# Optimization experiments

Hardware: AMD Instinct MI355X
Metric: run time of the kernel (lower is better)

The kernel has to match this reference:

```python
import jax, jax.numpy as jnp
import numpy as np

UNITS = 65
BATCH = 50
SEQ = 8192


def setup_inputs() -> dict:
    key = jax.random.key(0)
    ks = jax.random.split(key, 6)
    x = jax.random.normal(ks[0], (BATCH, SEQ, UNITS), dtype=jnp.float32)
    # Single shared LSTM cell (same cell object reused for all 3 stacked layers)
    W = jax.random.normal(ks[1], (UNITS, 4 * UNITS), dtype=jnp.float32) * 0.1
    U = jax.random.normal(ks[2], (UNITS, 4 * UNITS), dtype=jnp.float32) * 0.1
    b = jax.random.normal(ks[3], (4 * UNITS,), dtype=jnp.float32) * 0.1
    # Dense output projection 65 -> 65
    Wd = jax.random.normal(ks[4], (UNITS, UNITS), dtype=jnp.float32) * 0.1
    bd = jax.random.normal(ks[5], (UNITS,), dtype=jnp.float32) * 0.1
    return {"x": x, "W": W, "U": U, "b": b, "Wd": Wd, "bd": bd}


def _lstm_cell(x_t, h, c, W, U, b):
    # Keras LSTMCell: gates in order i, f, g(candidate), o
    z = x_t @ W + h @ U + b                      # [B, 4*units]
    i, f, g, o = jnp.split(z, 4, axis=-1)
    i = jax.nn.sigmoid(i)
    f = jax.nn.sigmoid(f)
    g = jnp.tanh(g)
    o = jax.nn.sigmoid(o)
    c_new = f * c + i * g
    h_new = o * jnp.tanh(c_new)
    return h_new, c_new


def reference(x, W, U, b, Wd, bd):
    B = x.shape[0]
    zeros = jnp.zeros((B, UNITS), dtype=x.dtype)
    init = (zeros, zeros, zeros, zeros, zeros, zeros)  # (h1,c1,h2,c2,h3,c3)

    def step(carry, x_t):
        h1, c1, h2, c2, h3, c3 = carry
        h1, c1 = _lstm_cell(x_t, h1, c1, W, U, b)  # layer 1 (shared weights)
        h2, c2 = _lstm_cell(h1, h2, c2, W, U, b)   # layer 2 (shared weights)
        h3, c3 = _lstm_cell(h2, h3, c3, W, U, b)   # layer 3 (shared weights)
        return (h1, c1, h2, c2, h3, c3), h3

    xs = jnp.swapaxes(x, 0, 1)                   # [T, B, 65]
    _, ys = jax.lax.scan(step, init, xs)         # ys: [T, B, 65]
    ys = jnp.swapaxes(ys, 0, 1)                  # [B, T, 65]
    out = ys @ Wd + bd                           # dense projection to vocab 65
    return out
```

## Files before the change

### kernel.cpp

```cpp
#include <hip/hip_runtime.h>

#define UNITS 65
#define SEQ   8192
#define BATCH 50

__device__ __forceinline__ float frcp(float x){ return __builtin_amdgcn_rcpf(x); }
__device__ __forceinline__ float fsigmoid(float x){ return frcp(1.0f + __expf(-x)); }
__device__ __forceinline__ float ftanh(float x){
    float e2 = __expf(2.0f * x);
    return 1.0f - 2.0f * frcp(e2 + 1.0f);
}

template<int CTRL>
__device__ __forceinline__ float dppadd(float x){
    int t = __builtin_amdgcn_update_dpp(0, __float_as_int(x), CTRL, 0xF, 0xF, true);
    return x + __int_as_float(t);
}
template<int CTRL>
__device__ __forceinline__ float dppmov(float x){
    int t = __builtin_amdgcn_update_dpp(0, __float_as_int(x), CTRL, 0xF, 0xF, true);
    return __int_as_float(t);
}
__device__ __forceinline__ float red4_all(float x){
    x = dppadd<0xB1>(x);
    x = dppadd<0x4E>(x);
    return x;
}
__device__ __forceinline__ float swzadd_xor4(float x){
    int t = __builtin_amdgcn_ds_swizzle(__float_as_int(x), 0x101F);
    return x + __int_as_float(t);
}
__device__ __forceinline__ float red8_all(float x){
    return swzadd_xor4(red4_all(x));
}
__device__ __forceinline__ float red16_lane15(float x){
    x = dppadd<0x111>(x);
    x = dppadd<0x112>(x);
    x = dppadd<0x114>(x);
    x = dppadd<0x118>(x);
    return x;
}
__device__ __forceinline__ void bar_lds(){
    asm volatile("s_waitcnt lgkmcnt(0)\n\ts_barrier" ::: "memory");
}
__device__ __forceinline__ float rdlane(float v, int l){
    return __int_as_float(__builtin_amdgcn_readlane(__float_as_int(v), l));
}

__device__ __forceinline__ int inpos8(int k){
    return (k < 112) ? ((k >> 4) * 20 + (k & 15)) : (140 + (k - 112));
}
__device__ __forceinline__ float wrow(const float* W, const float* U, int k, int c){
    return (k < 65) ? W[k * 260 + c] : U[(k - 65) * 260 + c];
}


#define LAYERB(aI, aF, aG, aO, CST, ...) do {                                  \
    float rI_ = red8_all(aI), rF_ = red8_all(aF);                              \
    float rG_ = red8_all(aG), rO_ = red8_all(aO);                              \
    float z_ = ((gate == 0) ? rI_ : (gate == 1) ? rF_ : (gate == 2) ? rG_ : rO_) + breg; \
    float sg_ = frcp(1.0f + __expf(-sk * z_));                                 \
    float g_  = fmaf(sk, sg_, dk);                                             \
    float gi_ = dppmov<0x00>(g_);                                              \
    float gf_ = dppmov<0x55>(g_);                                              \
    float gg_ = dppmov<0xAA>(g_);                                              \
    float cn_ = fmaf(gf_, CST, gi_ * gg_);                                     \
    float hn_ = g_ * ftanh(cn_);                                               \
    if (wr) { CST = cn_; __VA_ARGS__; }                                        \
} while (0)

#define STEP(L0, L1, L2, VB, NB) do {                                          \
    const float* __restrict__ vbase = (VB);                                    \
    float*       __restrict__ nbase = (NB);                                    \
          \
    float xq1 = 0.0f, ex1 = 0.0f;                                              \
    if (L0) {                                                                  \
        const int tl_ = (s + 2 < SEQ) ? (s + 2) : (SEQ - 1);                   \
        if (wr) xq1 = xrow[(size_t)tl_ * UNITS + j];                           \
        if (wave == 1 && lane == 0) ex1 = xrow[(size_t)tl_ * UNITS + 64];      \
    }                                                                          \
             \
    const float* vp0_ = vbase + k8 * 20;                                       \
    const float* vp1_ = vbase + 160 + k8 * 20;                                 \
    const float* vp2_ = vbase + 320 + k8 * 20;                                 \
    float aI0=0,aF0=0,aG0=0,aO0=0, aI1=0,aF1=0,aG1=0,aO1=0,                    \
          aI2=0,aF2=0,aG2=0,aO2=0;                                             \
    _Pragma("unroll")                                                          \
    for (int q4_ = 0; q4_ < 4; ++q4_) {                                        \
        float4 f0_, f1_, f2_;                                                  \
        if (L0) f0_ = *(const float4*)(vp0_ + 4 * q4_);                        \
        if (L1) f1_ = *(const float4*)(vp1_ + 4 * q4_);                        \
        if (L2) f2_ = *(const float4*)(vp2_ + 4 * q4_);                        \
        _Pragma("unroll")                                                      \
        for (int r_ = 0; r_ < 4; ++r_) {                                       \
            const int kk = 4 * q4_ + r_;                                       \
            if (L0) { float s0_ = (&f0_.x)[r_];                                \
                aI0=fmaf(s0_,wI[kk],aI0); aF0=fmaf(s0_,wF[kk],aF0);            \
                aG0=fmaf(s0_,wG[kk],aG0); aO0=fmaf(s0_,wO[kk],aO0); }          \
            if (L1) { float s1_ = (&f1_.x)[r_];                                \
                aI1=fmaf(s1_,wI[kk],aI1); aF1=fmaf(s1_,wF[kk],aF1);            \
                aG1=fmaf(s1_,wG[kk],aG1); aO1=fmaf(s1_,wO[kk],aO1); }          \
            if (L2) { float s2_ = (&f2_.x)[r_];                                \
                aI2=fmaf(s2_,wI[kk],aI2); aF2=fmaf(s2_,wF[kk],aF2);            \
                aG2=fmaf(s2_,wG[kk],aG2); aO2=fmaf(s2_,wO[kk],aO2); }          \
        }                                                                      \
    }                                                                          \
    {           \
        float2 t0_, t1_, t2_;                                                  \
        if (L0) t0_ = *(const float2*)(vp0_ + 16);                             \
        if (L1) t1_ = *(const float2*)(vp1_ + 16);                             \
        if (L2) t2_ = *(const float2*)(vp2_ + 16);                             \
        _Pragma("unroll")                                                      \
        for (int r_ = 0; r_ < 2; ++r_) {                                       \
            const int kk = 16 + r_;                                            \
            if (L0) { float s0_ = (&t0_.x)[r_];                                \
                aI0=fmaf(s0_,wI[kk],aI0); aF0=fmaf(s0_,wF[kk],aF0);            \
                aG0=fmaf(s0_,wG[kk],aG0); aO0=fmaf(s0_,wO[kk],aO0); }          \
            if (L1) { float s1_ = (&t1_.x)[r_];                                \
                aI1=fmaf(s1_,wI[kk],aI1); aF1=fmaf(s1_,wF[kk],aF1);            \
                aG1=fmaf(s1_,wG[kk],aG1); aO1=fmaf(s1_,wO[kk],aO1); }          \
            if (L2) { float s2_ = (&t2_.x)[r_];                                \
                aI2=fmaf(s2_,wI[kk],aI2); aF2=fmaf(s2_,wF[kk],aF2);            \
                aG2=fmaf(s2_,wG[kk],aG2); aO2=fmaf(s2_,wO[kk],aO2); }          \
        }                                                                      \
    }                                                                          \
          \
    const bool act64_ = (wave == 1) ? (bool)(L0)                               \
                      : (wave == 2) ? (bool)(L1)                               \
                      : (wave == 3) ? (bool)(L2) : false;                      \
    float a64_ = 0.0f;                                                         \
    if (act64_) {                                                              \
        const float* vm_ = vbase + ml * 160;                                   \
        float4 uA_ = *(const float4*)(vm_ + p64);                              \
        float4 uB_ = *(const float4*)(vm_ + p64 + 4);                          \
        float  uex_ = (i64 < 2) ? vm_[156 + i64] : 0.0f;                       \
        a64_ = uA_.x * w64[0];                                                 \
        a64_ = fmaf(uA_.y, w64[1], a64_); a64_ = fmaf(uA_.z, w64[2], a64_);    \
        a64_ = fmaf(uA_.w, w64[3], a64_); a64_ = fmaf(uB_.x, w64[4], a64_);    \
        a64_ = fmaf(uB_.y, w64[5], a64_); a64_ = fmaf(uB_.z, w64[6], a64_);    \
        a64_ = fmaf(uB_.w, w64[7], a64_); a64_ = fmaf(uex_, w64x, a64_);       \
        a64_ = red16_lane15(a64_);                                             \
    }                                                                          \
                                            \
    if (L0) LAYERB(aI0, aF0, aG0, aO0, c1,                                     \
                   nbase[ipH] = hn_; nbase[160 + ipI] = hn_);                  \
    if (L1) LAYERB(aI1, aF1, aG1, aO1, c2,                                     \
                   nbase[160 + ipH] = hn_; nbase[320 + ipI] = hn_);            \
    if (L2) LAYERB(aI2, aF2, aG2, aO2, c3,                                     \
                   nbase[320 + ipH] = hn_;                                     \
                   orow[(size_t)(s - 2) * UNITS + j] = hn_);                   \
    if (L0) { if (wr) { nbase[ipI] = xq0; xq0 = xq1; } }                       \
                               \
    if (act64_) {                                                              \
        float zi_ = rdlane(a64_, 15) + b64i;                                   \
        float zf_ = rdlane(a64_, 31) + b64f;                                   \
        float zg_ = rdlane(a64_, 47) + b64g;                                   \
        float zo_ = rdlane(a64_, 63) + b64o;                                   \
        float gi4_ = fsigmoid(zi_), gf4_ = fsigmoid(zf_);                      \
        float gg4_ = ftanh(zg_),    go4_ = fsigmoid(zo_);                      \
        float cn64_ = fmaf(gf4_, c64, gi4_ * gg4_);                            \
        float hn64_ = go4_ * ftanh(cn64_);                                     \
        c64 = cn64_;                                                           \
        if (lane == 0) {                                                       \
            nbase[ml * 160 + 157] = hn64_;                  \
            if (wave <= 2) nbase[(ml + 1) * 160 + 80] = hn64_;    \
            else orow[(size_t)(s - 2) * UNITS + 64] = hn64_;                   \
        }                                                                      \
        if (wave == 1) { if (lane == 0) nbase[80] = ex0; ex0 = ex1; }          \
    }                                                                          \
    bar_lds();                                                                 \
} while (0)

__global__ __launch_bounds__(512, 2)
void lstm3_kernel(const float* __restrict__ x, const float* __restrict__ W,
                  const float* __restrict__ U, const float* __restrict__ b,
                  float* __restrict__ out)
{
    const int e    = blockIdx.x;
    const int tid  = threadIdx.x;
    const int wave = tid >> 6, lane = tid & 63;
    const int k8   = lane & 7, ul = lane >> 3;
    const int j    = wave * 8 + ul;
    const int gate = k8 & 3;
    const bool wr  = (k8 == 7);

    __shared__ __attribute__((aligned(16))) float vbuf[2][3][160];

    float wI[18], wF[18], wG[18], wO[18];
    #pragma unroll
    for (int kk = 0; kk < 18; ++kk) {
        const int  k   = 16 * k8 + kk;
        const bool val = (kk < 16) || (k8 == 7);
        wI[kk] = val ? wrow(W, U, k, j)       : 0.0f;
        wF[kk] = val ? wrow(W, U, k, 65  + j) : 0.0f;
        wG[kk] = val ? wrow(W, U, k, 130 + j) : 0.0f;
        wO[kk] = val ? wrow(W, U, k, 195 + j) : 0.0f;
    }
    const float breg = b[gate * 65 + j];
    const float sk   = (gate == 2) ? 2.0f : 1.0f;
    const float dk   = 1.0f - sk;

    const int i64 = lane & 15, g64 = lane >> 4;
    const int p64 = (i64 >> 1) * 20 + 8 * (i64 & 1);
    float w64[8], w64x;
    {
        const int c64c = g64 * 65 + 64;
        #pragma unroll
        for (int r = 0; r < 8; ++r) w64[r] = wrow(W, U, 8 * i64 + r, c64c);
        w64x = (i64 < 2) ? wrow(W, U, 128 + i64, c64c) : 0.0f;
    }
    const float b64i = b[64], b64f = b[129], b64g = b[194], b64o = b[259];
    const int ml = (wave >= 1 && wave <= 3) ? (wave - 1) : 0;

    float c1 = 0, c2 = 0, c3 = 0, c64 = 0;

    const float* xrow = x   + (size_t)e * SEQ * UNITS;
    float*       orow = out + (size_t)e * SEQ * UNITS;
    const int ipI = inpos8(j), ipH = inpos8(65 + j);

    for (int i = tid; i < 2 * 3 * 160; i += 512) ((float*)&vbuf[0][0][0])[i] = 0.0f;
    __syncthreads();
    if (wr)  vbuf[0][0][ipI] = xrow[j];
    if (wave == 1 && lane == 0) vbuf[0][0][80] = xrow[64];
    __syncthreads();

    float xq0 = 0, ex0 = 0;
    if (wr) xq0 = xrow[UNITS + j];
    if (wave == 1 && lane == 0) ex0 = xrow[UNITS + 64];

    float* const vb0 = &vbuf[0][0][0];
    float* const vb1 = &vbuf[1][0][0];
    int s = 0;
    STEP(1, 0, 0, vb0, vb1); ++s;
    STEP(1, 1, 0, vb1, vb0); ++s;
    for (; s < SEQ - 1; ) {
        STEP(1, 1, 1, vb0, vb1); ++s;
        STEP(1, 1, 1, vb1, vb0); ++s;
    }
    STEP(0, 1, 1, vb0, vb1); ++s;
    STEP(0, 0, 1, vb1, vb0);
}

__global__ __launch_bounds__(256)
void dense_kernel(float* __restrict__ io,
                  const float* __restrict__ Wd,
                  const float* __restrict__ bd)
{
    __shared__ __attribute__((aligned(16))) float wS[65 * 68];
    __shared__ float bS[65];
    for (int i = threadIdx.x; i < 65 * 65; i += 256) {
        int r = i / 65, c = i - r * 65;
        wS[r * 68 + c] = Wd[i];
    }
    if (threadIdx.x < 65) bS[threadIdx.x] = bd[threadIdx.x];
    __syncthreads();

    const size_t row  = (size_t)blockIdx.x * 256 + threadIdx.x;
    const size_t base = row * 65;

    float r[65];
    #pragma unroll
    for (int k = 0; k < 65; ++k) r[k] = io[base + k];

    for (int ct = 0; ct < 16; ++ct) {
        const int c = ct * 4;
        float a0 = bS[c], a1 = bS[c + 1], a2 = bS[c + 2], a3 = bS[c + 3];
        #pragma unroll
        for (int k = 0; k < 65; ++k) {
            const float4 wv = *reinterpret_cast<const float4*>(&wS[k * 68 + c]);
            a0 += r[k] * wv.x;
            a1 += r[k] * wv.y;
            a2 += r[k] * wv.z;
            a3 += r[k] * wv.w;
        }
        io[base + c]     = a0;
        io[base + c + 1] = a1;
        io[base + c + 2] = a2;
        io[base + c + 3] = a3;
    }
    float a = bS[64];
    #pragma unroll
    for (int k = 0; k < 65; ++k) a += r[k] * wS[k * 68 + 64];
    io[base + 64] = a;
}

extern "C" void kernel_launch(void* const* d_in, const int* in_sizes, int n_in,
                              void* d_out, int out_size, void* d_ws, size_t ws_size,
                              hipStream_t stream)
{
    const float* x  = (const float*)d_in[0];
    const float* W  = (const float*)d_in[1];
    const float* U  = (const float*)d_in[2];
    const float* b  = (const float*)d_in[3];
    const float* Wd = (const float*)d_in[4];
    const float* bd = (const float*)d_in[5];
    float* out = (float*)d_out;

    hipLaunchKernelGGL(lstm3_kernel, dim3(BATCH), dim3(512), 0, stream, x, W, U, b, out);
    hipLaunchKernelGGL(dense_kernel, dim3(1600), dim3(256), 0, stream, out, Wd, bd);
}
```

Measured before the change: 14.51 ms.

## Split LSTM dot products across 16 lanes with 1024-thread blocks

Each hidden unit's 130-long dot product is now split over 16 lanes with about 10 inputs each, instead of 8 lanes with about 18, and the block grows to 1024 threads (16 waves, 4 units per wave). The cross-lane reduction becomes a DPP-only tree (quad adds plus row_shr adds) that replaces the ds_swizzle, and the gate broadcast uses row shifts. The LDS layout is repacked to 12-float strides with 192 floats per layer. This shortens the serial FMA chain on each timestep's critical path, at the cost of twice as many waves meeting at every per-step barrier and more reduction steps.

```diff
diff --git a/kernel.cpp b/kernel.cpp
--- a/kernel.cpp
+++ b/kernel.cpp
@@ -3,6 +3,7 @@
 #define UNITS 65
 #define SEQ   8192
 #define BATCH 50
+#define LAYER 192
 
 __device__ __forceinline__ float frcp(float x){ return __builtin_amdgcn_rcpf(x); }
 __device__ __forceinline__ float fsigmoid(float x){ return frcp(1.0f + __expf(-x)); }
@@ -25,13 +26,6 @@
     x = dppadd<0xB1>(x);
     x = dppadd<0x4E>(x);
     return x;
-}
-__device__ __forceinline__ float swzadd_xor4(float x){
-    int t = __builtin_amdgcn_ds_swizzle(__float_as_int(x), 0x101F);
-    return x + __int_as_float(t);
-}
-__device__ __forceinline__ float red8_all(float x){
-    return swzadd_xor4(red4_all(x));
 }
 __device__ __forceinline__ float red16_lane15(float x){
     x = dppadd<0x111>(x);
@@ -47,8 +41,8 @@
     return __int_as_float(__builtin_amdgcn_readlane(__float_as_int(v), l));
 }
 
-__device__ __forceinline__ int inpos8(int k){
-    return (k < 112) ? ((k >> 4) * 20 + (k & 15)) : (140 + (k - 112));
+__device__ __forceinline__ int inpos16(int k){
+    return (k < 120) ? ((k >> 3) * 12 + (k & 7)) : (180 + (k - 120));
 }
 __device__ __forceinline__ float wrow(const float* W, const float* U, int k, int c){
     return (k < 65) ? W[k * 260 + c] : U[(k - 65) * 260 + c];
@@ -56,14 +50,17 @@
 
 
 #define LAYERB(aI, aF, aG, aO, CST, ...) do {                                  \
-    float rI_ = red8_all(aI), rF_ = red8_all(aF);                              \
-    float rG_ = red8_all(aG), rO_ = red8_all(aO);                              \
-    float z_ = ((gate == 0) ? rI_ : (gate == 1) ? rF_ : (gate == 2) ? rG_ : rO_) + breg; \
+    float qI_ = red4_all(aI), qF_ = red4_all(aF);                              \
+    float qG_ = red4_all(aG), qO_ = red4_all(aO);                              \
+    float z_ = ((gsel == 0) ? qI_ : (gsel == 1) ? qF_ : (gsel == 2) ? qG_ : qO_); \
+    z_ = dppadd<0x114>(z_);                        \
+    z_ = dppadd<0x118>(z_);              \
+    z_ += breg;                                                                \
     float sg_ = frcp(1.0f + __expf(-sk * z_));                                 \
-    float g_  = fmaf(sk, sg_, dk);                                             \
-    float gi_ = dppmov<0x00>(g_);                                              \
-    float gf_ = dppmov<0x55>(g_);                                              \
-    float gg_ = dppmov<0xAA>(g_);                                              \
+    float g_  = fmaf(sk, sg_, dk);                \
+    float gi_ = dppmov<0x113>(g_);                   \
+    float gf_ = dppmov<0x112>(g_);                   \
+    float gg_ = dppmov<0x111>(g_);                   \
     float cn_ = fmaf(gf_, CST, gi_ * gg_);                                     \
     float hn_ = g_ * ftanh(cn_);                                               \
     if (wr) { CST = cn_; __VA_ARGS__; }                                        \
@@ -80,13 +77,13 @@
         if (wave == 1 && lane == 0) ex1 = xrow[(size_t)tl_ * UNITS + 64];      \
     }                                                                          \
              \
-    const float* vp0_ = vbase + k8 * 20;                                       \
-    const float* vp1_ = vbase + 160 + k8 * 20;                                 \
-    const float* vp2_ = vbase + 320 + k8 * 20;                                 \
+    const float* vp0_ = vbase + k16 * 12;                                      \
+    const float* vp1_ = vbase + LAYER + k16 * 12;                              \
+    const float* vp2_ = vbase + 2 * LAYER + k16 * 12;                          \
     float aI0=0,aF0=0,aG0=0,aO0=0, aI1=0,aF1=0,aG1=0,aO1=0,                    \
           aI2=0,aF2=0,aG2=0,aO2=0;                                             \
     _Pragma("unroll")                                                          \
-    for (int q4_ = 0; q4_ < 4; ++q4_) {                                        \
+    for (int q4_ = 0; q4_ < 2; ++q4_) {                                        \
         float4 f0_, f1_, f2_;                                                  \
         if (L0) f0_ = *(const float4*)(vp0_ + 4 * q4_);                        \
         if (L1) f1_ = *(const float4*)(vp1_ + 4 * q4_);                        \
@@ -107,12 +104,12 @@
     }                                                                          \
     {           \
         float2 t0_, t1_, t2_;                                                  \
-        if (L0) t0_ = *(const float2*)(vp0_ + 16);                             \
-        if (L1) t1_ = *(const float2*)(vp1_ + 16);                             \
-        if (L2) t2_ = *(const float2*)(vp2_ + 16);                             \
+        if (L0) t0_ = *(const float2*)(vp0_ + 8);                              \
+        if (L1) t1_ = *(const float2*)(vp1_ + 8);                              \
+        if (L2) t2_ = *(const float2*)(vp2_ + 8);                              \
         _Pragma("unroll")                                                      \
         for (int r_ = 0; r_ < 2; ++r_) {                                       \
-            const int kk = 16 + r_;                                            \
+            const int kk = 8 + r_;                                             \
             if (L0) { float s0_ = (&t0_.x)[r_];                                \
                 aI0=fmaf(s0_,wI[kk],aI0); aF0=fmaf(s0_,wF[kk],aF0);            \
                 aG0=fmaf(s0_,wG[kk],aG0); aO0=fmaf(s0_,wO[kk],aO0); }          \
@@ -130,10 +127,10 @@
                       : (wave == 3) ? (bool)(L2) : false;                      \
     float a64_ = 0.0f;                                                         \
     if (act64_) {                                                              \
-        const float* vm_ = vbase + ml * 160;                                   \
+        const float* vm_ = vbase + ml * LAYER;                                 \
         float4 uA_ = *(const float4*)(vm_ + p64);                              \
         float4 uB_ = *(const float4*)(vm_ + p64 + 4);                          \
-        float  uex_ = (i64 < 2) ? vm_[156 + i64] : 0.0f;                       \
+        float  uex_ = (i64 < 2) ? vm_[188 + i64] : 0.0f;                       \
         a64_ = uA_.x * w64[0];                                                 \
         a64_ = fmaf(uA_.y, w64[1], a64_); a64_ = fmaf(uA_.z, w64[2], a64_);    \
         a64_ = fmaf(uA_.w, w64[3], a64_); a64_ = fmaf(uB_.x, w64[4], a64_);    \
@@ -143,11 +140,11 @@
     }                                                                          \
                                             \
     if (L0) LAYERB(aI0, aF0, aG0, aO0, c1,                                     \
-                   nbase[ipH] = hn_; nbase[160 + ipI] = hn_);                  \
+                   nbase[ipH] = hn_; nbase[LAYER + ipI] = hn_);                \
     if (L1) LAYERB(aI1, aF1, aG1, aO1, c2,                                     \
-                   nbase[160 + ipH] = hn_; nbase[320 + ipI] = hn_);            \
+                   nbase[LAYER + ipH] = hn_; nbase[2 * LAYER + ipI] = hn_);    \
     if (L2) LAYERB(aI2, aF2, aG2, aO2, c3,                                     \
-                   nbase[320 + ipH] = hn_;                                     \
+                   nbase[2 * LAYER + ipH] = hn_;                               \
                    orow[(size_t)(s - 2) * UNITS + j] = hn_);                   \
     if (L0) { if (wr) { nbase[ipI] = xq0; xq0 = xq1; } }                       \
                                \
@@ -162,16 +159,16 @@
         float hn64_ = go4_ * ftanh(cn64_);                                     \
         c64 = cn64_;                                                           \
         if (lane == 0) {                                                       \
-            nbase[ml * 160 + 157] = hn64_;                  \
-            if (wave <= 2) nbase[(ml + 1) * 160 + 80] = hn64_;    \
+            nbase[ml * LAYER + 189] = hn64_;                     \
+            if (wave <= 2) nbase[(ml + 1) * LAYER + 96] = hn64_;  \
             else orow[(size_t)(s - 2) * UNITS + 64] = hn64_;                   \
         }                                                                      \
-        if (wave == 1) { if (lane == 0) nbase[80] = ex0; ex0 = ex1; }          \
+        if (wave == 1) { if (lane == 0) nbase[96] = ex0; ex0 = ex1; }          \
     }                                                                          \
     bar_lds();                                                                 \
 } while (0)
 
-__global__ __launch_bounds__(512, 2)
+__global__ __launch_bounds__(1024, 4)
 void lstm3_kernel(const float* __restrict__ x, const float* __restrict__ W,
                   const float* __restrict__ U, const float* __restrict__ b,
                   float* __restrict__ out)
@@ -179,29 +176,29 @@
     const int e    = blockIdx.x;
     const int tid  = threadIdx.x;
     const int wave = tid >> 6, lane = tid & 63;
-    const int k8   = lane & 7, ul = lane >> 3;
-    const int j    = wave * 8 + ul;
-    const int gate = k8 & 3;
-    const bool wr  = (k8 == 7);
-
-    __shared__ __attribute__((aligned(16))) float vbuf[2][3][160];
-
-    float wI[18], wF[18], wG[18], wO[18];
+    const int k16  = lane & 15, ul = lane >> 4;
+    const int j    = wave * 4 + ul;
+    const int gsel = k16 & 3;
+    const bool wr  = (k16 == 15);
+
+    __shared__ __attribute__((aligned(16))) float vbuf[2][3][LAYER];
+
+    float wI[10], wF[10], wG[10], wO[10];
     #pragma unroll
-    for (int kk = 0; kk < 18; ++kk) {
-        const int  k   = 16 * k8 + kk;
-        const bool val = (kk < 16) || (k8 == 7);
+    for (int kk = 0; kk < 10; ++kk) {
+        const int  k   = 8 * k16 + kk;
+        const bool val = (kk < 8) || (k16 == 15);
         wI[kk] = val ? wrow(W, U, k, j)       : 0.0f;
         wF[kk] = val ? wrow(W, U, k, 65  + j) : 0.0f;
         wG[kk] = val ? wrow(W, U, k, 130 + j) : 0.0f;
         wO[kk] = val ? wrow(W, U, k, 195 + j) : 0.0f;
     }
-    const float breg = b[gate * 65 + j];
-    const float sk   = (gate == 2) ? 2.0f : 1.0f;
+    const float breg = b[gsel * 65 + j];
+    const float sk   = (gsel == 2) ? 2.0f : 1.0f;
     const float dk   = 1.0f - sk;
 
     const int i64 = lane & 15, g64 = lane >> 4;
-    const int p64 = (i64 >> 1) * 20 + 8 * (i64 & 1);
+    const int p64 = i64 * 12;
     float w64[8], w64x;
     {
         const int c64c = g64 * 65 + 64;
@@ -216,12 +213,12 @@
 
     const float* xrow = x   + (size_t)e * SEQ * UNITS;
     float*       orow = out + (size_t)e * SEQ * UNITS;
-    const int ipI = inpos8(j), ipH = inpos8(65 + j);
-
-    for (int i = tid; i < 2 * 3 * 160; i += 512) ((float*)&vbuf[0][0][0])[i] = 0.0f;
+    const int ipI = inpos16(j), ipH = inpos16(65 + j);
+
+    for (int i = tid; i < 2 * 3 * LAYER; i += 1024) ((float*)&vbuf[0][0][0])[i] = 0.0f;
     __syncthreads();
     if (wr)  vbuf[0][0][ipI] = xrow[j];
-    if (wave == 1 && lane == 0) vbuf[0][0][80] = xrow[64];
+    if (wave == 1 && lane == 0) vbuf[0][0][96] = xrow[64];
     __syncthreads();
 
     float xq0 = 0, ex0 = 0;
@@ -296,6 +293,6 @@
     const float* bd = (const float*)d_in[5];
     float* out = (float*)d_out;
 
-    hipLaunchKernelGGL(lstm3_kernel, dim3(BATCH), dim3(512), 0, stream, x, W, U, b, out);
+    hipLaunchKernelGGL(lstm3_kernel, dim3(BATCH), dim3(1024), 0, stream, x, W, U, b, out);
     hipLaunchKernelGGL(dense_kernel, dim3(1600), dim3(256), 0, stream, out, Wd, bd);
 }
```

Result: slower. 19.36 ms (+33.4%).
